# Kernel tuning notes

Measured on AMD Instinct MI355X. Metric: run time of the kernel, lower is better.

## Reference

```python
import jax, jax.numpy as jnp
import numpy as np

NUM_RULES = 256
IN_F = 2048
OUT_F = 2048
RANK = 8
BLOCK = 64
NUM_BLOCKS = min(IN_F, OUT_F) // BLOCK  # 32
SHARED_RANK = int(round(np.sqrt(min(IN_F, OUT_F))))  # 45
N = 16384


def setup_inputs() -> dict:
    key = jax.random.key(0)
    ks = jax.random.split(key, 7)
    x = jax.random.normal(ks[0], (N, IN_F), dtype=jnp.float32)
    rule_ids = jax.random.randint(ks[1], (N,), 0, NUM_RULES, dtype=jnp.int32)
    shared_in = jax.random.normal(ks[2], (IN_F, SHARED_RANK), dtype=jnp.float32) * (1.0 / np.sqrt(IN_F))
    shared_out = jax.random.normal(ks[3], (SHARED_RANK, OUT_F), dtype=jnp.float32) * (1.0 / np.sqrt(SHARED_RANK))
    rule_in = jax.random.normal(ks[4], (NUM_RULES, BLOCK, RANK), dtype=jnp.float32) * (1.0 / np.sqrt(BLOCK))
    rule_out = jax.random.normal(ks[5], (NUM_RULES, RANK, BLOCK), dtype=jnp.float32) * (1.0 / np.sqrt(RANK))
    rule_block_logits = jax.random.normal(ks[6], (NUM_RULES, NUM_BLOCKS), dtype=jnp.float32) * (1.0 / np.sqrt(NUM_BLOCKS))
    return {"x": x, "rule_ids": rule_ids, "shared_in": shared_in, "shared_out": shared_out,
            "rule_in": rule_in, "rule_out": rule_out, "rule_block_logits": rule_block_logits}


def reference(x, rule_ids, shared_in, shared_out, rule_in, rule_out, rule_block_logits):
    # Shared low-rank path: [N, in] @ [in, r] @ [r, out]
    base_out = (x @ shared_in) @ shared_out  # [N, OUT_F]

    total = NUM_BLOCKS * BLOCK
    x_blocks = x[:, :total].reshape(-1, NUM_BLOCKS, BLOCK)  # [N, B, bs]

    # Per-token gather of rule adapter params. This is mathematically
    # identical to the torch sort/pad/bmm/scatter path (zero padding
    # contributes zero), expressed as a dense gather + batched einsum.
    r_in = rule_in[rule_ids]    # [N, bs, RANK]
    r_out = rule_out[rule_ids]  # [N, RANK, bs]
    hidden = jnp.einsum('nbs,nsr->nbr', x_blocks, r_in)     # [N, B, RANK]
    adapter = jnp.einsum('nbr,nrs->nbs', hidden, r_out)     # [N, B, bs]

    # Block selector softmax with temperature 1/sqrt(num_blocks)
    inv_temp = jnp.sqrt(jnp.float32(NUM_BLOCKS))
    sel = jax.nn.softmax(rule_block_logits[rule_ids] * inv_temp, axis=-1)  # [N, B]
    weighted = (adapter * sel[:, :, None]).reshape(-1, total)  # [N, total]

    adapter_full = jnp.zeros_like(base_out).at[:, :total].set(weighted.astype(base_out.dtype))
    return base_out + adapter_full
```

## Files before the change

kernel.cpp:

```cpp
#include <hip/hip_runtime.h>
#include <hip/hip_bf16.h>
#include <math.h>

#define NTOK  16384
#define INF   2048
#define OUTF  2048
#define SR    45
#define RANK  8
#define BLK   64
#define NBLK  32
#define NRULE 256
#define NHIST 32
#define MAXSLOT (NTOK + NRULE * 15)
#define NTILE16 (MAXSLOT / 16)
#define NTILE32 (MAXSLOT / 32)

typedef __attribute__((ext_vector_type(8))) short bf16x8;
typedef __attribute__((ext_vector_type(4))) float f32x4;
typedef __attribute__((ext_vector_type(4))) short s16x4;

#define MFMA __builtin_amdgcn_mfma_f32_16x16x32_bf16
#define SBAR() __builtin_amdgcn_sched_barrier(0)

__device__ inline short f2bs(float f) {
    __hip_bfloat16 h = __float2bfloat16(f);
    return *reinterpret_cast<short*>(&h);
}
__device__ inline bf16x8 cvt8(const float4& a, const float4& b) {
    bf16x8 r;
    r[0] = f2bs(a.x); r[1] = f2bs(a.y); r[2] = f2bs(a.z); r[3] = f2bs(a.w);
    r[4] = f2bs(b.x); r[5] = f2bs(b.y); r[6] = f2bs(b.z); r[7] = f2bs(b.w);
    return r;
}

__global__ void kprep_a(const int* __restrict__ rule_ids,
                        const float* __restrict__ shared_in,
                        const float* __restrict__ shared_out,
                        const float* __restrict__ rule_in,
                        const float* __restrict__ rule_out,
                        unsigned short* __restrict__ ssb,
                        unsigned short* __restrict__ sob,
                        unsigned short* __restrict__ rinf,
                        unsigned short* __restrict__ rof,
                        int* __restrict__ ghist_part,
                        int* __restrict__ perm_p,
                        int* __restrict__ srid_p)
{
    if (blockIdx.x < 128) {
        const int tid = blockIdx.x * 256 + threadIdx.x;
        const int stride = 128 * 256;
        for (int idx = tid; idx < 64 * 3 * 512; idx += stride) {
            int ch = idx / 1536, rem = idx - ch * 1536;
            int nf = rem / 512;
            int l = (rem >> 3) & 63, j = idx & 7;
            int k = ch * 32 + ((l >> 4) << 3) + j;
            int col = nf * 16 + (l & 15);
            ssb[idx] = (col < SR) ? (unsigned short)f2bs(shared_in[(size_t)k * SR + col]) : 0;
        }
        for (int idx = tid; idx < 128 * 2 * 512; idx += stride) {
            int CF = idx >> 10;
            int kc = (idx >> 9) & 1;
            int l = (idx >> 3) & 63, j = idx & 7;
            int k = kc * 32 + ((l >> 4) << 3) + j;
            int col = CF * 16 + (l & 15);
            sob[idx] = (k < SR) ? (unsigned short)f2bs(shared_out[(size_t)k * OUTF + col]) : 0;
        }
        for (int idx = tid; idx < NRULE * 2 * 512; idx += stride) {
            int rid = idx >> 10;
            int half = (idx >> 9) & 1;
            int l = (idx >> 3) & 63, j = idx & 7;
            int r = l & 15;
            int s = half * 32 + ((l >> 4) << 3) + j;
            rinf[idx] = (r < RANK) ? (unsigned short)f2bs(rule_in[(size_t)rid * 512 + s * RANK + r]) : 0;
        }
        for (int idx = tid; idx < NRULE * 4 * 512; idx += stride) {
            int rid = idx >> 11;
            int cf = (idx >> 9) & 3;
            int l = (idx >> 3) & 63, j = idx & 7;
            int k = ((l >> 4) << 3) + j;
            int c = cf * 16 + (l & 15);
            rof[idx] = (k < RANK) ? (unsigned short)f2bs(rule_out[(size_t)rid * 512 + k * BLK + c]) : 0;
        }
    } else {
        __shared__ int lh[NRULE];
        const int tid = threadIdx.x;
        const int hb = blockIdx.x - 128;
        lh[tid] = 0;
        __syncthreads();
        const int base = hb * 512;
        atomicAdd(&lh[rule_ids[base + tid]], 1);
        atomicAdd(&lh[rule_ids[base + 256 + tid]], 1);
        __syncthreads();
        ghist_part[hb * NRULE + tid] = lh[tid];
        for (int j = tid; j < MAXSLOT / 32; j += 256) {
            int idx = hb * (MAXSLOT / 32) + j;
            perm_p[idx] = -1;
            srid_p[idx] = 0;
        }
    }
}

__global__ void kprep_scan(const int* __restrict__ ghist_part,
                           const float* __restrict__ logits,
                           int* __restrict__ gcnt,
                           int* __restrict__ srid_p,
                           float* __restrict__ sel_t,
                           int* __restrict__ ntot)
{
    __shared__ int sc[NRULE];
    const int tid = threadIdx.x;
    int h = 0;
#pragma unroll
    for (int b = 0; b < NHIST; ++b) h += ghist_part[b * NRULE + tid];
    const int pd = (h + 15) & ~15;
    sc[tid] = pd;
    for (int off = 1; off < NRULE; off <<= 1) {
        __syncthreads();
        int v = (tid >= off) ? sc[tid - off] : 0;
        __syncthreads();
        sc[tid] += v;
    }
    __syncthreads();
    const int excl = sc[tid] - pd;
    gcnt[tid] = excl;
    for (int q = h; q < pd; ++q) srid_p[excl + q] = tid;
    if (tid == NRULE - 1) *ntot = sc[tid];
    const float invT = 5.65685424949238f;
    const float* __restrict__ lg = logits + (size_t)tid * NBLK;
    float m = -1e30f;
    for (int b = 0; b < NBLK; ++b) m = fmaxf(m, lg[b] * invT);
    float s = 0.0f;
    for (int b = 0; b < NBLK; ++b) s += expf(lg[b] * invT - m);
    const float inv = 1.0f / s;
    for (int b = 0; b < NBLK; ++b)
        sel_t[(size_t)tid * NBLK + b] = expf(lg[b] * invT - m) * inv;
}

__global__ void kprep_scatter(const int* __restrict__ rule_ids,
                              int* __restrict__ gcnt,
                              int* __restrict__ perm_p,
                              int* __restrict__ srid_p)
{
    const int i = blockIdx.x * 256 + threadIdx.x;
    const int r = rule_ids[i];
    const int p = atomicAdd(&gcnt[r], 1);
    perm_p[p] = i;
    srid_p[p] = r;
}

__global__ __launch_bounds__(256, 4)
void k1(const float* __restrict__ x,
        const int* __restrict__ perm_p,
        const int* __restrict__ srid_p,
        const unsigned short* __restrict__ ssb,
        const unsigned short* __restrict__ rinf,
        const float* __restrict__ sel_t,
        const int* __restrict__ ntot,
        unsigned short* __restrict__ t_bf,
        unsigned short* __restrict__ hs)
{
    __shared__ __align__(16) float tred[4][16][52];
    __shared__ __align__(16) unsigned short hs_lds[16 * 264];

    const int slot0 = blockIdx.x * 16;
    if (slot0 >= *ntot) return;

    const int tid  = threadIdx.x;
    const int lane = tid & 63;
    const int w    = tid >> 6;
    const int row_l = lane & 15, grp = lane >> 4;

    const int rid_u = __builtin_amdgcn_readfirstlane(srid_p[slot0]);
    int tok = perm_p[slot0 + row_l];
    if (tok < 0) tok = 0;

    const float* __restrict__ xr = x + (size_t)tok * INF + w * 512 + (grp << 3);
    const unsigned short* __restrict__ sbase =
        ssb + (size_t)(w * 16) * 1536 + lane * 8;
    const bf16x8 ri0 = *(const bf16x8*)(rinf + ((size_t)rid_u * 2 + 0) * 512 + lane * 8);
    const bf16x8 ri1 = *(const bf16x8*)(rinf + ((size_t)rid_u * 2 + 1) * 512 + lane * 8);

    f32x4 aT0 = {0.f, 0.f, 0.f, 0.f};
    f32x4 aT1 = {0.f, 0.f, 0.f, 0.f};
    f32x4 aT2 = {0.f, 0.f, 0.f, 0.f};
    f32x4 aH  = {0.f, 0.f, 0.f, 0.f};

    float4 xa[5][2];
    bf16x8 wr[3][3];
#pragma unroll
    for (int s_ = 0; s_ < 4; ++s_) {
        xa[s_][0] = *(const float4*)(xr + s_ * 32);
        xa[s_][1] = *(const float4*)(xr + s_ * 32 + 4);
    }
#pragma unroll
    for (int s_ = 0; s_ < 2; ++s_) {
        const unsigned short* sp = sbase + (size_t)s_ * 1536;
        wr[s_][0] = *(const bf16x8*)(sp);
        wr[s_][1] = *(const bf16x8*)(sp + 512);
        wr[s_][2] = *(const bf16x8*)(sp + 1024);
    }
    SBAR();

#pragma unroll
    for (int c = 0; c < 16; ++c) {
        if (c < 12) {
            xa[(c + 4) % 5][0] = *(const float4*)(xr + (c + 4) * 32);
            xa[(c + 4) % 5][1] = *(const float4*)(xr + (c + 4) * 32 + 4);
        }
        if (c < 14) {
            const unsigned short* sp = sbase + (size_t)(c + 2) * 1536;
            wr[(c + 2) % 3][0] = *(const bf16x8*)(sp);
            wr[(c + 2) % 3][1] = *(const bf16x8*)(sp + 512);
            wr[(c + 2) % 3][2] = *(const bf16x8*)(sp + 1024);
        }
        SBAR();
        const bf16x8 af = cvt8(xa[c % 5][0], xa[c % 5][1]);
        aT0 = MFMA(af, wr[c % 3][0], aT0, 0, 0, 0);
        aT1 = MFMA(af, wr[c % 3][1], aT1, 0, 0, 0);
        aT2 = MFMA(af, wr[c % 3][2], aT2, 0, 0, 0);
        aH  = MFMA(af, (c & 1) ? ri1 : ri0, aH, 0, 0, 0);
        if (c & 1) {
            const int b = w * 8 + (c >> 1);
            const float sel = sel_t[(size_t)rid_u * NBLK + b];
            if (row_l < RANK) {
#pragma unroll
                for (int q = 0; q < 4; ++q)
                    hs_lds[((grp << 2) + q) * 264 + b * 8 + row_l] =
                        (unsigned short)f2bs(aH[q] * sel);
            }
            aH[0] = 0.f; aH[1] = 0.f; aH[2] = 0.f; aH[3] = 0.f;
        }
        SBAR();
    }

#pragma unroll
    for (int q = 0; q < 4; ++q) {
        const int sl = (grp << 2) + q;
        tred[w][sl][row_l]      = aT0[q];
        tred[w][sl][16 + row_l] = aT1[q];
        tred[w][sl][32 + row_l] = aT2[q];
    }
    __syncthreads();
    {
        const int sl = tid >> 4;
        const int c0 = (tid & 15) << 2;
        s16x4 v = {0, 0, 0, 0};
        if (c0 < 48) {
#pragma unroll
            for (int j = 0; j < 4; ++j) {
                const float s = tred[0][sl][c0 + j] + tred[1][sl][c0 + j]
                              + tred[2][sl][c0 + j] + tred[3][sl][c0 + j];
                v[j] = f2bs(s);
            }
        }
        *(s16x4*)(t_bf + ((size_t)(slot0 + sl)) * 64 + c0) = v;
    }
#pragma unroll
    for (int u = 0; u < 2; ++u) {
        const int f = tid + (u << 8);
        const int sl = f >> 5, j8 = f & 31;
        *(bf16x8*)(hs + ((size_t)(slot0 + sl)) * 256 + j8 * 8) =
            *(const bf16x8*)(&hs_lds[sl * 264 + j8 * 8]);
    }
}

__global__ __launch_bounds__(256, 4)
void k2(const unsigned short* __restrict__ t_bf,
        const unsigned short* __restrict__ hs,
        const int* __restrict__ perm_p,
        const int* __restrict__ srid_p,
        const unsigned short* __restrict__ sob,
        const unsigned short* __restrict__ rof,
        const int* __restrict__ ntot,
        float* __restrict__ dummy,
        float* __restrict__ out)
{
    const int bid  = blockIdx.x;
    const int xcd  = bid & 7;
    const int cq   = xcd >> 1;
    const int tile = ((bid >> 3) << 1) | (xcd & 1);
    const int slot0 = tile * 32;
    if (slot0 >= *ntot) return;

    const int tid  = threadIdx.x;
    const int lane = tid & 63;
    const int w    = tid >> 6;
    const int s    = w & 1;
    const int p    = w >> 1;
    const int row_l = lane & 15, grp = lane >> 4;
    const int slotbase = slot0 + s * 16;

    const int rid_u = __builtin_amdgcn_readfirstlane(srid_p[slotbase]);

    const unsigned short* __restrict__ tb =
        t_bf + ((size_t)(slotbase + row_l)) * 64 + (grp << 3);
    const bf16x8 at0 = *(const bf16x8*)(tb);
    const bf16x8 at1 = *(const bf16x8*)(tb + 32);

    bf16x8 rfv[4];
#pragma unroll
    for (int i = 0; i < 4; ++i)
        rfv[i] = *(const bf16x8*)(rof + ((size_t)rid_u * 4 + i) * 512 + lane * 8);

    const int4 pv = *(const int4*)(perm_p + slotbase + (grp << 2));
    float* const orow0 = (pv.x < 0) ? dummy : out + (size_t)pv.x * OUTF;
    float* const orow1 = (pv.y < 0) ? dummy : out + (size_t)pv.y * OUTF;
    float* const orow2 = (pv.z < 0) ? dummy : out + (size_t)pv.z * OUTF;
    float* const orow3 = (pv.w < 0) ? dummy : out + (size_t)pv.w * OUTF;

    const int CF0 = cq * 32 + p * 16;
    const unsigned short* __restrict__ sobw = sob + (size_t)CF0 * 1024 + lane * 8;
    const unsigned short* __restrict__ hsw  = hs + ((size_t)(slotbase + (lane & 15))) * 256;
    const int bb0 = CF0 >> 2;

    bf16x8 sb[4][2];
    bf16x8 ah[2];
    const bf16x8 zz = {0, 0, 0, 0, 0, 0, 0, 0};

#define LOADQ(SL, QI) do { \
        const unsigned short* _sp = sobw + (size_t)(QI) * 1024; \
        sb[SL][0] = *(const bf16x8*)(_sp); \
        sb[SL][1] = *(const bf16x8*)(_sp + 512); \
    } while (0)
#define LOADA(SL, BI) do { \
        ah[SL] = zz; \
        if (lane < 16) \
            ah[SL] = *(const bf16x8*)(hsw + (size_t)(bb0 + (BI)) * 8); \
    } while (0)

    LOADQ(0, 0); LOADQ(1, 1); LOADQ(2, 2);
    LOADA(0, 0);
    SBAR();

#pragma unroll
    for (int qi = 0; qi < 16; ++qi) {
        if (qi < 13) LOADQ((qi + 3) & 3, qi + 3);
        if ((qi & 3) == 0 && qi < 12) LOADA(((qi >> 2) + 1) & 1, (qi >> 2) + 1);
        SBAR();
        f32x4 acc = {0.f, 0.f, 0.f, 0.f};
        acc = MFMA(at0, sb[qi & 3][0], acc, 0, 0, 0);
        acc = MFMA(at1, sb[qi & 3][1], acc, 0, 0, 0);
        acc = MFMA(ah[(qi >> 2) & 1], rfv[qi & 3], acc, 0, 0, 0);
        const int col = ((CF0 + qi) << 4) + row_l;
        orow0[col] = acc[0];
        orow1[col] = acc[1];
        orow2[col] = acc[2];
        orow3[col] = acc[3];
        SBAR();
    }
#undef LOADQ
#undef LOADA
}

extern "C" void kernel_launch(void* const* d_in, const int* in_sizes, int n_in,
                              void* d_out, int out_size, void* d_ws, size_t ws_size,
                              hipStream_t stream)
{
    const float* x          = (const float*)d_in[0];
    const int*   rule_ids   = (const int*)  d_in[1];
    const float* shared_in  = (const float*)d_in[2];
    const float* shared_out = (const float*)d_in[3];
    const float* rule_in    = (const float*)d_in[4];
    const float* rule_out   = (const float*)d_in[5];
    const float* logits     = (const float*)d_in[6];
    float* out = (float*)d_out;

    char* p = (char*)d_ws;
    auto carve = [&p](size_t bytes) {
        char* r = p;
        p += (bytes + 255) & ~(size_t)255;
        return r;
    };
    int*            perm_p = (int*)carve(MAXSLOT * 4);
    int*            srid_p = (int*)carve(MAXSLOT * 4);
    unsigned short* ssb    = (unsigned short*)carve(64 * 3 * 512 * 2);
    unsigned short* sob    = (unsigned short*)carve(128 * 2 * 512 * 2);
    unsigned short* rinf   = (unsigned short*)carve((size_t)NRULE * 2 * 512 * 2);
    unsigned short* rof    = (unsigned short*)carve((size_t)NRULE * 4 * 512 * 2);
    float*          sel_t  = (float*)carve((size_t)NRULE * NBLK * 4);
    int*            ghistp = (int*)carve((size_t)NHIST * NRULE * 4);
    int*            gcnt   = (int*)carve(NRULE * 4);
    int*            ntot   = (int*)carve(4);
    float*          dummy  = (float*)carve((size_t)OUTF * 4);
    unsigned short* t_bf   = (unsigned short*)carve((size_t)MAXSLOT * 64 * 2);
    unsigned short* hs     = (unsigned short*)carve((size_t)MAXSLOT * 256 * 2);

    kprep_a<<<dim3(160), dim3(256), 0, stream>>>(
        rule_ids, shared_in, shared_out, rule_in, rule_out,
        ssb, sob, rinf, rof, ghistp, perm_p, srid_p);
    kprep_scan<<<dim3(1), dim3(256), 0, stream>>>(
        ghistp, logits, gcnt, srid_p, sel_t, ntot);
    kprep_scatter<<<dim3(64), dim3(256), 0, stream>>>(
        rule_ids, gcnt, perm_p, srid_p);
    k1<<<dim3(NTILE16), dim3(256), 0, stream>>>(
        x, perm_p, srid_p, ssb, rinf, sel_t, ntot, t_bf, hs);
    k2<<<dim3(NTILE32 * 4), dim3(256), 0, stream>>>(
        t_bf, hs, perm_p, srid_p, sob, rof, ntot, dummy, out);
}
```

Baseline: 106.0 us.

## Fuse down-projection and up-projection kernels into one kernel via LDS intermediates

Merges the two main kernels into a single 512-thread kernel that handles 32 slots per block. The shared-rank projection and per-rule hidden values stay in LDS instead of round-tripping through global scratch buffers, which removes one launch and that global traffic. Each block now writes all 2048 output columns for its tokens, where before the column range was split across four blocks. This cuts the grid size by a factor of four and lengthens each block's serial store loop, which risks lower parallelism and store throughput. Padding rows are now skipped with predicated stores instead of a dummy row.

```diff
diff --git a/kernel.cpp b/kernel.cpp
--- a/kernel.cpp
+++ b/kernel.cpp
@@ -12,7 +12,6 @@
 #define NRULE 256
 #define NHIST 32
 #define MAXSLOT (NTOK + NRULE * 15)
-#define NTILE16 (MAXSLOT / 16)
 #define NTILE32 (MAXSLOT / 32)
 
 typedef __attribute__((ext_vector_type(8))) short bf16x8;
@@ -148,138 +147,23 @@
     srid_p[p] = r;
 }
 
-__global__ __launch_bounds__(256, 4)
-void k1(const float* __restrict__ x,
-        const int* __restrict__ perm_p,
-        const int* __restrict__ srid_p,
-        const unsigned short* __restrict__ ssb,
-        const unsigned short* __restrict__ rinf,
-        const float* __restrict__ sel_t,
-        const int* __restrict__ ntot,
-        unsigned short* __restrict__ t_bf,
-        unsigned short* __restrict__ hs)
-{
-    __shared__ __align__(16) float tred[4][16][52];
-    __shared__ __align__(16) unsigned short hs_lds[16 * 264];
-
-    const int slot0 = blockIdx.x * 16;
-    if (slot0 >= *ntot) return;
-
-    const int tid  = threadIdx.x;
-    const int lane = tid & 63;
-    const int w    = tid >> 6;
-    const int row_l = lane & 15, grp = lane >> 4;
-
-    const int rid_u = __builtin_amdgcn_readfirstlane(srid_p[slot0]);
-    int tok = perm_p[slot0 + row_l];
-    if (tok < 0) tok = 0;
-
-    const float* __restrict__ xr = x + (size_t)tok * INF + w * 512 + (grp << 3);
-    const unsigned short* __restrict__ sbase =
-        ssb + (size_t)(w * 16) * 1536 + lane * 8;
-    const bf16x8 ri0 = *(const bf16x8*)(rinf + ((size_t)rid_u * 2 + 0) * 512 + lane * 8);
-    const bf16x8 ri1 = *(const bf16x8*)(rinf + ((size_t)rid_u * 2 + 1) * 512 + lane * 8);
-
-    f32x4 aT0 = {0.f, 0.f, 0.f, 0.f};
-    f32x4 aT1 = {0.f, 0.f, 0.f, 0.f};
-    f32x4 aT2 = {0.f, 0.f, 0.f, 0.f};
-    f32x4 aH  = {0.f, 0.f, 0.f, 0.f};
-
-    float4 xa[5][2];
-    bf16x8 wr[3][3];
-#pragma unroll
-    for (int s_ = 0; s_ < 4; ++s_) {
-        xa[s_][0] = *(const float4*)(xr + s_ * 32);
-        xa[s_][1] = *(const float4*)(xr + s_ * 32 + 4);
-    }
-#pragma unroll
-    for (int s_ = 0; s_ < 2; ++s_) {
-        const unsigned short* sp = sbase + (size_t)s_ * 1536;
-        wr[s_][0] = *(const bf16x8*)(sp);
-        wr[s_][1] = *(const bf16x8*)(sp + 512);
-        wr[s_][2] = *(const bf16x8*)(sp + 1024);
-    }
-    SBAR();
-
-#pragma unroll
-    for (int c = 0; c < 16; ++c) {
-        if (c < 12) {
-            xa[(c + 4) % 5][0] = *(const float4*)(xr + (c + 4) * 32);
-            xa[(c + 4) % 5][1] = *(const float4*)(xr + (c + 4) * 32 + 4);
-        }
-        if (c < 14) {
-            const unsigned short* sp = sbase + (size_t)(c + 2) * 1536;
-            wr[(c + 2) % 3][0] = *(const bf16x8*)(sp);
-            wr[(c + 2) % 3][1] = *(const bf16x8*)(sp + 512);
-            wr[(c + 2) % 3][2] = *(const bf16x8*)(sp + 1024);
-        }
-        SBAR();
-        const bf16x8 af = cvt8(xa[c % 5][0], xa[c % 5][1]);
-        aT0 = MFMA(af, wr[c % 3][0], aT0, 0, 0, 0);
-        aT1 = MFMA(af, wr[c % 3][1], aT1, 0, 0, 0);
-        aT2 = MFMA(af, wr[c % 3][2], aT2, 0, 0, 0);
-        aH  = MFMA(af, (c & 1) ? ri1 : ri0, aH, 0, 0, 0);
-        if (c & 1) {
-            const int b = w * 8 + (c >> 1);
-            const float sel = sel_t[(size_t)rid_u * NBLK + b];
-            if (row_l < RANK) {
-#pragma unroll
-                for (int q = 0; q < 4; ++q)
-                    hs_lds[((grp << 2) + q) * 264 + b * 8 + row_l] =
-                        (unsigned short)f2bs(aH[q] * sel);
-            }
-            aH[0] = 0.f; aH[1] = 0.f; aH[2] = 0.f; aH[3] = 0.f;
-        }
-        SBAR();
-    }
-
-#pragma unroll
-    for (int q = 0; q < 4; ++q) {
-        const int sl = (grp << 2) + q;
-        tred[w][sl][row_l]      = aT0[q];
-        tred[w][sl][16 + row_l] = aT1[q];
-        tred[w][sl][32 + row_l] = aT2[q];
-    }
-    __syncthreads();
-    {
-        const int sl = tid >> 4;
-        const int c0 = (tid & 15) << 2;
-        s16x4 v = {0, 0, 0, 0};
-        if (c0 < 48) {
-#pragma unroll
-            for (int j = 0; j < 4; ++j) {
-                const float s = tred[0][sl][c0 + j] + tred[1][sl][c0 + j]
-                              + tred[2][sl][c0 + j] + tred[3][sl][c0 + j];
-                v[j] = f2bs(s);
-            }
-        }
-        *(s16x4*)(t_bf + ((size_t)(slot0 + sl)) * 64 + c0) = v;
-    }
-#pragma unroll
-    for (int u = 0; u < 2; ++u) {
-        const int f = tid + (u << 8);
-        const int sl = f >> 5, j8 = f & 31;
-        *(bf16x8*)(hs + ((size_t)(slot0 + sl)) * 256 + j8 * 8) =
-            *(const bf16x8*)(&hs_lds[sl * 264 + j8 * 8]);
-    }
-}
-
-__global__ __launch_bounds__(256, 4)
-void k2(const unsigned short* __restrict__ t_bf,
-        const unsigned short* __restrict__ hs,
-        const int* __restrict__ perm_p,
-        const int* __restrict__ srid_p,
-        const unsigned short* __restrict__ sob,
-        const unsigned short* __restrict__ rof,
-        const int* __restrict__ ntot,
-        float* __restrict__ dummy,
-        float* __restrict__ out)
-{
-    const int bid  = blockIdx.x;
-    const int xcd  = bid & 7;
-    const int cq   = xcd >> 1;
-    const int tile = ((bid >> 3) << 1) | (xcd & 1);
-    const int slot0 = tile * 32;
+__global__ __launch_bounds__(512, 4)
+void kmain(const float* __restrict__ x,
+           const int* __restrict__ perm_p,
+           const int* __restrict__ srid_p,
+           const unsigned short* __restrict__ ssb,
+           const unsigned short* __restrict__ sob,
+           const unsigned short* __restrict__ rinf,
+           const unsigned short* __restrict__ rof,
+           const float* __restrict__ sel_t,
+           const int* __restrict__ ntot,
+           float* __restrict__ out)
+{
+    __shared__ __align__(16) float tred[8][16][52];
+    __shared__ __align__(16) unsigned short hs_lds[2][16][264];
+    __shared__ __align__(16) unsigned short t_bf[32][72];
+
+    const int slot0 = blockIdx.x * 32;
     if (slot0 >= *ntot) return;
 
     const int tid  = threadIdx.x;
@@ -291,31 +175,118 @@
     const int slotbase = slot0 + s * 16;
 
     const int rid_u = __builtin_amdgcn_readfirstlane(srid_p[slotbase]);
-
-    const unsigned short* __restrict__ tb =
-        t_bf + ((size_t)(slotbase + row_l)) * 64 + (grp << 3);
-    const bf16x8 at0 = *(const bf16x8*)(tb);
-    const bf16x8 at1 = *(const bf16x8*)(tb + 32);
-
-    bf16x8 rfv[4];
-#pragma unroll
-    for (int i = 0; i < 4; ++i)
-        rfv[i] = *(const bf16x8*)(rof + ((size_t)rid_u * 4 + i) * 512 + lane * 8);
-
-    const int4 pv = *(const int4*)(perm_p + slotbase + (grp << 2));
-    float* const orow0 = (pv.x < 0) ? dummy : out + (size_t)pv.x * OUTF;
-    float* const orow1 = (pv.y < 0) ? dummy : out + (size_t)pv.y * OUTF;
-    float* const orow2 = (pv.z < 0) ? dummy : out + (size_t)pv.z * OUTF;
-    float* const orow3 = (pv.w < 0) ? dummy : out + (size_t)pv.w * OUTF;
-
-    const int CF0 = cq * 32 + p * 16;
-    const unsigned short* __restrict__ sobw = sob + (size_t)CF0 * 1024 + lane * 8;
-    const unsigned short* __restrict__ hsw  = hs + ((size_t)(slotbase + (lane & 15))) * 256;
-    const int bb0 = CF0 >> 2;
-
-    bf16x8 sb[4][2];
-    bf16x8 ah[2];
-    const bf16x8 zz = {0, 0, 0, 0, 0, 0, 0, 0};
+    int tok = perm_p[slotbase + row_l];
+    if (tok < 0) tok = 0;
+
+    {
+        const float* __restrict__ xr = x + (size_t)tok * INF + p * 512 + (grp << 3);
+        const unsigned short* __restrict__ sbase =
+            ssb + (size_t)(p * 16) * 1536 + lane * 8;
+        const bf16x8 ri0 = *(const bf16x8*)(rinf + ((size_t)rid_u * 2 + 0) * 512 + lane * 8);
+        const bf16x8 ri1 = *(const bf16x8*)(rinf + ((size_t)rid_u * 2 + 1) * 512 + lane * 8);
+
+        f32x4 aT0 = {0.f, 0.f, 0.f, 0.f};
+        f32x4 aT1 = {0.f, 0.f, 0.f, 0.f};
+        f32x4 aT2 = {0.f, 0.f, 0.f, 0.f};
+        f32x4 aH  = {0.f, 0.f, 0.f, 0.f};
+
+        float4 xa[4][2];
+        bf16x8 wr[3][3];
+#pragma unroll
+        for (int s_ = 0; s_ < 3; ++s_) {
+            xa[s_][0] = *(const float4*)(xr + s_ * 32);
+            xa[s_][1] = *(const float4*)(xr + s_ * 32 + 4);
+        }
+#pragma unroll
+        for (int s_ = 0; s_ < 2; ++s_) {
+            const unsigned short* sp = sbase + (size_t)s_ * 1536;
+            wr[s_][0] = *(const bf16x8*)(sp);
+            wr[s_][1] = *(const bf16x8*)(sp + 512);
+            wr[s_][2] = *(const bf16x8*)(sp + 1024);
+        }
+        SBAR();
+
+#pragma unroll
+        for (int c = 0; c < 16; ++c) {
+            if (c < 13) {
+                xa[(c + 3) & 3][0] = *(const float4*)(xr + (c + 3) * 32);
+                xa[(c + 3) & 3][1] = *(const float4*)(xr + (c + 3) * 32 + 4);
+            }
+            if (c < 14) {
+                const unsigned short* sp = sbase + (size_t)(c + 2) * 1536;
+                wr[(c + 2) % 3][0] = *(const bf16x8*)(sp);
+                wr[(c + 2) % 3][1] = *(const bf16x8*)(sp + 512);
+                wr[(c + 2) % 3][2] = *(const bf16x8*)(sp + 1024);
+            }
+            SBAR();
+            const bf16x8 af = cvt8(xa[c & 3][0], xa[c & 3][1]);
+            aT0 = MFMA(af, wr[c % 3][0], aT0, 0, 0, 0);
+            aT1 = MFMA(af, wr[c % 3][1], aT1, 0, 0, 0);
+            aT2 = MFMA(af, wr[c % 3][2], aT2, 0, 0, 0);
+            aH  = MFMA(af, (c & 1) ? ri1 : ri0, aH, 0, 0, 0);
+            if (c & 1) {
+                const int b = p * 8 + (c >> 1);
+                const float sel = sel_t[(size_t)rid_u * NBLK + b];
+                if (row_l < RANK) {
+#pragma unroll
+                    for (int q = 0; q < 4; ++q)
+                        hs_lds[s][(grp << 2) + q][b * 8 + row_l] =
+                            (unsigned short)f2bs(aH[q] * sel);
+                }
+                aH[0] = 0.f; aH[1] = 0.f; aH[2] = 0.f; aH[3] = 0.f;
+            }
+            SBAR();
+        }
+
+#pragma unroll
+        for (int q = 0; q < 4; ++q) {
+            const int tk = (grp << 2) + q;
+            tred[w][tk][row_l]      = aT0[q];
+            tred[w][tk][16 + row_l] = aT1[q];
+            tred[w][tk][32 + row_l] = aT2[q];
+        }
+    }
+    __syncthreads();
+    {
+        const int sl = tid >> 4;
+        const int st = sl >> 4, tk = sl & 15;
+        const int c0 = (tid & 15) << 2;
+        s16x4 v = {0, 0, 0, 0};
+        if (c0 < 48) {
+#pragma unroll
+            for (int j = 0; j < 4; ++j) {
+                const float sm = tred[st][tk][c0 + j] + tred[2 + st][tk][c0 + j]
+                               + tred[4 + st][tk][c0 + j] + tred[6 + st][tk][c0 + j];
+                v[j] = f2bs(sm);
+            }
+        }
+        *(s16x4*)(&t_bf[sl][c0]) = v;
+    }
+    __syncthreads();
+    SBAR();
+
+    {
+        const bf16x8 at0 = *(const bf16x8*)(&t_bf[s * 16 + row_l][grp << 3]);
+        const bf16x8 at1 = *(const bf16x8*)(&t_bf[s * 16 + row_l][32 + (grp << 3)]);
+
+        bf16x8 rfv[4];
+#pragma unroll
+        for (int i = 0; i < 4; ++i)
+            rfv[i] = *(const bf16x8*)(rof + ((size_t)rid_u * 4 + i) * 512 + lane * 8);
+
+        const int4 pv = *(const int4*)(perm_p + slotbase + (grp << 2));
+        float* const orow0 = out + (size_t)pv.x * OUTF;
+        float* const orow1 = out + (size_t)pv.y * OUTF;
+        float* const orow2 = out + (size_t)pv.z * OUTF;
+        float* const orow3 = out + (size_t)pv.w * OUTF;
+
+        const int CF0 = p * 32;
+        const int bb0 = p * 8;
+        const unsigned short* __restrict__ sobw = sob + (size_t)CF0 * 1024 + lane * 8;
+
+        bf16x8 sb[4][2];
+        bf16x8 ah[2];
+        const bf16x8 zz = {0, 0, 0, 0, 0, 0, 0, 0};
 
 #define LOADQ(SL, QI) do { \
         const unsigned short* _sp = sobw + (size_t)(QI) * 1024; \
@@ -325,31 +296,32 @@
 #define LOADA(SL, BI) do { \
         ah[SL] = zz; \
         if (lane < 16) \
-            ah[SL] = *(const bf16x8*)(hsw + (size_t)(bb0 + (BI)) * 8); \
+            ah[SL] = *(const bf16x8*)(&hs_lds[s][lane][(bb0 + (BI)) * 8]); \
     } while (0)
 
-    LOADQ(0, 0); LOADQ(1, 1); LOADQ(2, 2);
-    LOADA(0, 0);
-    SBAR();
-
-#pragma unroll
-    for (int qi = 0; qi < 16; ++qi) {
-        if (qi < 13) LOADQ((qi + 3) & 3, qi + 3);
-        if ((qi & 3) == 0 && qi < 12) LOADA(((qi >> 2) + 1) & 1, (qi >> 2) + 1);
+        LOADQ(0, 0); LOADQ(1, 1); LOADQ(2, 2);
+        LOADA(0, 0);
         SBAR();
-        f32x4 acc = {0.f, 0.f, 0.f, 0.f};
-        acc = MFMA(at0, sb[qi & 3][0], acc, 0, 0, 0);
-        acc = MFMA(at1, sb[qi & 3][1], acc, 0, 0, 0);
-        acc = MFMA(ah[(qi >> 2) & 1], rfv[qi & 3], acc, 0, 0, 0);
-        const int col = ((CF0 + qi) << 4) + row_l;
-        orow0[col] = acc[0];
-        orow1[col] = acc[1];
-        orow2[col] = acc[2];
-        orow3[col] = acc[3];
-        SBAR();
-    }
+
+#pragma unroll
+        for (int qi = 0; qi < 32; ++qi) {
+            if (qi < 29) LOADQ((qi + 3) & 3, qi + 3);
+            if ((qi & 3) == 0 && qi < 28) LOADA(((qi >> 2) + 1) & 1, (qi >> 2) + 1);
+            SBAR();
+            f32x4 acc = {0.f, 0.f, 0.f, 0.f};
+            acc = MFMA(at0, sb[qi & 3][0], acc, 0, 0, 0);
+            acc = MFMA(at1, sb[qi & 3][1], acc, 0, 0, 0);
+            acc = MFMA(ah[(qi >> 2) & 1], rfv[qi & 3], acc, 0, 0, 0);
+            const int col = ((CF0 + qi) << 4) + row_l;
+            if (pv.x >= 0) orow0[col] = acc[0];
+            if (pv.y >= 0) orow1[col] = acc[1];
+            if (pv.z >= 0) orow2[col] = acc[2];
+            if (pv.w >= 0) orow3[col] = acc[3];
+            SBAR();
+        }
 #undef LOADQ
 #undef LOADA
+    }
 }
 
 extern "C" void kernel_launch(void* const* d_in, const int* in_sizes, int n_in,
@@ -381,9 +353,6 @@
     int*            ghistp = (int*)carve((size_t)NHIST * NRULE * 4);
     int*            gcnt   = (int*)carve(NRULE * 4);
     int*            ntot   = (int*)carve(4);
-    float*          dummy  = (float*)carve((size_t)OUTF * 4);
-    unsigned short* t_bf   = (unsigned short*)carve((size_t)MAXSLOT * 64 * 2);
-    unsigned short* hs     = (unsigned short*)carve((size_t)MAXSLOT * 256 * 2);
 
     kprep_a<<<dim3(160), dim3(256), 0, stream>>>(
         rule_ids, shared_in, shared_out, rule_in, rule_out,
@@ -392,8 +361,6 @@
         ghistp, logits, gcnt, srid_p, sel_t, ntot);
     kprep_scatter<<<dim3(64), dim3(256), 0, stream>>>(
         rule_ids, gcnt, perm_p, srid_p);
-    k1<<<dim3(NTILE16), dim3(256), 0, stream>>>(
-        x, perm_p, srid_p, ssb, rinf, sel_t, ntot, t_bf, hs);
-    k2<<<dim3(NTILE32 * 4), dim3(256), 0, stream>>>(
-        t_bf, hs, perm_p, srid_p, sob, rof, ntot, dummy, out);
-}
+    kmain<<<dim3(NTILE32), dim3(512), 0, stream>>>(
+        x, perm_p, srid_p, ssb, sob, rinf, rof, sel_t, ntot, out);
+}
```

New measurement: 117.9 us. 1.11x slower.
